# Performance work log

Hardware: AMD Instinct MI355X
Metric: run time of the kernel (lower is better)

Reference implementation:

```python
import jax, jax.numpy as jnp
import numpy as np

D_IN = 1024
D_OUT = 1024
D_BOT = 512


def setup_inputs() -> dict:
    key = jax.random.key(0)
    ks = jax.random.split(key, 16)
    B, Sq, Skv = 8, 2048, 2048

    def lin(k, fan_in, fan_out):
        kw, kb = jax.random.split(k)
        bound = 1.0 / np.sqrt(fan_in)
        W = jax.random.uniform(kw, (fan_in, fan_out), jnp.float32, -bound, bound)
        b = jax.random.uniform(kb, (fan_out,), jnp.float32, -bound, bound)
        return W, b

    W1, b1 = lin(ks[0], D_IN, D_IN)
    W2, b2 = lin(ks[1], D_IN, D_BOT)
    W3, b3 = lin(ks[2], D_BOT, D_IN)
    W4, b4 = lin(ks[3], D_IN, D_IN)
    Wq, bq = lin(ks[4], D_IN, D_OUT)
    Wk, bk = lin(ks[5], D_IN, D_OUT)
    Wv, bv = lin(ks[6], D_IN, D_OUT)

    x = jax.random.normal(ks[7], (B, Sq, D_IN), jnp.float32)
    y = jax.random.normal(ks[8], (B, Skv, D_IN), jnp.float32)
    return {
        "x": x, "y": y,
        "W1": W1, "b1": b1, "W2": W2, "b2": b2,
        "W3": W3, "b3": b3, "W4": W4, "b4": b4,
        "Wq": Wq, "bq": bq, "Wk": Wk, "bk": bk, "Wv": Wv, "bv": bv,
    }


def reference(x, y, W1, b1, W2, b2, W3, b3, W4, b4, Wq, bq, Wk, bk, Wv, bv):
    # 4-layer MLP with ReLU after every linear
    h = jax.nn.relu(x @ W1 + b1)
    h = jax.nn.relu(h @ W2 + b2)
    h = jax.nn.relu(h @ W3 + b3)
    h = jax.nn.relu(h @ W4 + b4)
    # cross-attention projections
    q = h @ Wq + bq          # [B, Sq, D_OUT]
    k = y @ Wk + bk          # [B, Skv, D_OUT]
    v = y @ Wv + bv          # [B, Skv, D_OUT]
    scale = 1.0 / jnp.sqrt(jnp.float32(q.shape[-1]))
    scores = jnp.einsum('bqd,bkd->bqk', q, k) * scale  # [B, Sq, Skv]
    attn_w = jax.nn.softmax(scores, axis=-1)
    out = jnp.einsum('bqk,bkd->bqd', attn_w, v)
    return out
```

## Files before the change

kernel.cpp:

```cpp
#include <hip/hip_runtime.h>
#include <stdint.h>


typedef __attribute__((ext_vector_type(8))) short bf16x8;
typedef __attribute__((ext_vector_type(4))) float f32x4;
typedef __attribute__((ext_vector_type(8))) unsigned short u16x8;

#define LOG2E_F 1.44269504088896f
#define LN2_F   0.69314718055995f

__device__ __forceinline__ float bf2f(unsigned short u) {
    return __uint_as_float(((unsigned int)u) << 16);
}
__device__ __forceinline__ unsigned short f2bf(float f) {
    unsigned int u = __float_as_uint(f);
    unsigned int r = (u + 0x7fffu + ((u >> 16) & 1u)) >> 16;
    return (unsigned short)r;
}

__device__ __forceinline__ void async16(const void* g, void* l) {
    __builtin_amdgcn_global_load_lds(
        (const __attribute__((address_space(1))) unsigned int*)g,
        (__attribute__((address_space(3))) unsigned int*)l,
        16, 0, 0);
}

__global__ __launch_bounds__(64) void detect_dtype(
    const unsigned short* __restrict__ w, int* __restrict__ flag)
{
    const int t = threadIdx.x;
    int cnt = 0;
    for (int i = t; i < 4096; i += 64) {
        const unsigned e = (w[i] >> 7) & 0xFF;
        cnt += (e >= 140) ? 1 : 0;
    }
#pragma unroll
    for (int off = 32; off; off >>= 1) cnt += __shfl_xor(cnt, off, 64);
    if (t == 0) flag[0] = (cnt >= 8) ? 1 : 0;
}

__global__ __launch_bounds__(256) void conv_bias_all(
    const void* b1, const void* b2, const void* b3, const void* b4,
    const void* bq, const void* bk, const void* bv,
    float* __restrict__ out, const int* __restrict__ flag)
{
    const int i = blockIdx.x * 256 + threadIdx.x;
    const int slot = i >> 10, idx = i & 1023;
    if (slot == 1 && idx >= 512) return;
    const void* src = (slot == 0) ? b1 : (slot == 1) ? b2 : (slot == 2) ? b3 :
                      (slot == 3) ? b4 : (slot == 4) ? bq : (slot == 5) ? bk : bv;
    out[i] = (*flag) ? ((const float*)src)[idx]
                     : bf2f(((const unsigned short*)src)[idx]);
}

__device__ __forceinline__ void wt_body(
    const void* in, unsigned short* out, int R, int C, int f)
{
    __shared__ unsigned short tile[32][33];
    const int bc = blockIdx.x * 32;
    const int br = blockIdx.y * 32;
    const int x = threadIdx.x & 31;
    const int y = threadIdx.x >> 5;
#pragma unroll
    for (int i = 0; i < 4; i++) {
        const int r = y + i * 8;
        unsigned short v;
        if (f) v = f2bf(((const float*)in)[(size_t)(br + r) * C + bc + x]);
        else   v = ((const unsigned short*)in)[(size_t)(br + r) * C + bc + x];
        tile[r][x] = v;
    }
    __syncthreads();
#pragma unroll
    for (int i = 0; i < 4; i++) {
        const int r = y + i * 8;
        out[(size_t)(bc + r) * R + br + x] = tile[x][r];
    }
}

__global__ __launch_bounds__(256) void conv_weight_t7(
    const void* i0, unsigned short* o0, const void* i1, unsigned short* o1,
    const void* i2, unsigned short* o2, const void* i3, unsigned short* o3,
    const void* i4, unsigned short* o4, const void* i5, unsigned short* o5,
    const void* i6, unsigned short* o6, const int* flag)
{
    const int z = blockIdx.z;
    if (z == 5) {
        if (blockIdx.x >= 16) return;
        wt_body(i5, o5, 1024, 512, *flag);
        return;
    }
    if (z == 6) {
        if (blockIdx.y >= 16) return;
        wt_body(i6, o6, 512, 1024, *flag);
        return;
    }
    const void* in = (z == 0) ? i0 : (z == 1) ? i1 : (z == 2) ? i2 : (z == 3) ? i3 : i4;
    unsigned short* out = (z == 0) ? o0 : (z == 1) ? o1 : (z == 2) ? o2 : (z == 3) ? o3 : o4;
    wt_body(in, out, 1024, 1024, *flag);
}

__global__ __launch_bounds__(256) void conv_to_bf16(
    const void* __restrict__ in, unsigned short* __restrict__ out,
    int n, const int* __restrict__ flag)
{
    const int i = (blockIdx.x * 256 + threadIdx.x) * 8;
    if (i >= n) return;
    if (*flag) {
        const float4* p = (const float4*)((const float*)in + i);
        const float4 a = p[0], b = p[1];
        u16x8 o;
        o[0] = f2bf(a.x); o[1] = f2bf(a.y); o[2] = f2bf(a.z); o[3] = f2bf(a.w);
        o[4] = f2bf(b.x); o[5] = f2bf(b.y); o[6] = f2bf(b.z); o[7] = f2bf(b.w);
        *(u16x8*)(out + i) = o;
    } else {
        *(u16x8*)(out + i) = *(const u16x8*)((const unsigned short*)in + i);
    }
}

__global__ __launch_bounds__(256) void write_out(
    const unsigned short* __restrict__ src, void* __restrict__ dst,
    int n, const int* __restrict__ flag)
{
    const int i = (blockIdx.x * 256 + threadIdx.x) * 8;
    if (i >= n) return;
    const u16x8 v = *(const u16x8*)(src + i);
    if (*flag) {
        float4 a, b;
        a.x = bf2f(v[0]); a.y = bf2f(v[1]); a.z = bf2f(v[2]); a.w = bf2f(v[3]);
        b.x = bf2f(v[4]); b.y = bf2f(v[5]); b.z = bf2f(v[6]); b.w = bf2f(v[7]);
        float4* p = (float4*)((float*)dst + i);
        p[0] = a; p[1] = b;
    } else {
        *(u16x8*)((unsigned short*)dst + i) = v;
    }
}

template <int RELU, int BIAS, int OUTF, int SWZ>
__global__ __launch_bounds__(256, 2) void gemm_bt(
    const unsigned short* __restrict__ A, const unsigned short* __restrict__ B,
    const float* __restrict__ bias, void* __restrict__ C,
    int M, int N, int K, float alpha,
    long long sA, long long sB, long long sC, const int* __restrict__ flag)
{
    int bxi = blockIdx.x, byi = blockIdx.y;
    if (SWZ) {
        const int id = byi * gridDim.x + bxi;
        bxi = (id >> 3) % gridDim.x;
        byi = (id >> 3) / gridDim.x * 8 + (id & 7);
    }
    const int z = blockIdx.z;
    A += (size_t)z * (size_t)sA;
    B += (size_t)z * (size_t)sB;
    const size_t cofs = (size_t)z * (size_t)sC;

    const int bm = byi * 128;
    const int bn = bxi * 128;
    const int t = threadIdx.x;
    const int lane = t & 63;
    const int w = t >> 6;
    const int wr = (w >> 1) * 64;
    const int wc = (w & 1) * 64;

    __shared__ unsigned short sAt[128 * 32];
    __shared__ unsigned short sBt[128 * 32];

    f32x4 acc[4][4];
#pragma unroll
    for (int i = 0; i < 4; i++)
#pragma unroll
        for (int j = 0; j < 4; j++)
            acc[i][j] = (f32x4){0.f, 0.f, 0.f, 0.f};

    const int tr = t >> 2;
    const int tc = (t & 3) << 3;
    const unsigned short* ga = A + (size_t)(bm + tr) * K + tc;
    const unsigned short* gb = B + (size_t)(bn + tr) * K + tc;
    unsigned short* la = &sAt[tr * 32 + tc];
    unsigned short* lb = &sBt[tr * 32 + tc];

    const int am = wr + (lane & 15);
    const int bn_ = wc + (lane & 15);
    const int ak = (lane >> 4) * 8;

    for (int k0 = 0; k0 < K; k0 += 32) {
        async16(ga, la);
        async16(ga + (size_t)64 * K, la + 64 * 32);
        async16(gb, lb);
        async16(gb + (size_t)64 * K, lb + 64 * 32);
        ga += 32;
        gb += 32;
        __syncthreads();

        bf16x8 af[4], bfr[4];
#pragma unroll
        for (int i = 0; i < 4; i++)
            af[i] = *(const bf16x8*)&sAt[(am + i * 16) * 32 + ak];
#pragma unroll
        for (int j = 0; j < 4; j++)
            bfr[j] = *(const bf16x8*)&sBt[(bn_ + j * 16) * 32 + ak];
#pragma unroll
        for (int i = 0; i < 4; i++)
#pragma unroll
            for (int j = 0; j < 4; j++)
                acc[i][j] = __builtin_amdgcn_mfma_f32_16x16x32_bf16(
                    af[i], bfr[j], acc[i][j], 0, 0, 0);
        __syncthreads();
    }

    const int fl = OUTF ? *flag : 0;
#pragma unroll
    for (int i = 0; i < 4; i++) {
        const int row0 = bm + wr + i * 16 + (lane >> 4) * 4;
#pragma unroll
        for (int j = 0; j < 4; j++) {
            const int col = bn + wc + j * 16 + (lane & 15);
            float bc = 0.f;
            if (BIAS == 1) bc = bias[col];
#pragma unroll
            for (int r = 0; r < 4; r++) {
                float bv = bc;
                if (BIAS == 2) bv = bias[row0 + r];
                float vv = acc[i][j][r] * alpha + bv;
                if (RELU) vv = fmaxf(vv, 0.f);
                const size_t idx = cofs + (size_t)(row0 + r) * N + col;
                if (OUTF && fl) ((float*)C)[idx] = vv;
                else ((unsigned short*)C)[idx] = f2bf(vv);
            }
        }
    }
}

#define G10_STG(SOFS, KOFS) do {                                               \
    async16(gAs + (KOFS), dA + (SOFS));                                        \
    async16(gAs + (KOFS) + rk128, dA + (SOFS) + 4096);                         \
    async16(gBs + (KOFS), dB + (SOFS));                                        \
    async16(gBs + (KOFS) + rk128, dB + (SOFS) + 4096);                         \
} while (0)

template <int RELU, int BIAS, int OUTF, int SWZ, int STAT, int NORM>
__global__ __launch_bounds__(512, 2) void gemm8(
    const unsigned short* __restrict__ A, const unsigned short* __restrict__ B,
    const float* __restrict__ bias, void* __restrict__ C,
    int M, int N, int K, float alpha,
    long long sA, long long sB, long long sC, const int* __restrict__ flag,
    const float* __restrict__ ms, float* __restrict__ ps)
{
    extern __shared__ unsigned short lds[];
    int bxi = blockIdx.x, byi = blockIdx.y;
    if (SWZ) {
        const int id = byi * gridDim.x + bxi;
        bxi = (id >> 3) % gridDim.x;
        byi = (id >> 3) / gridDim.x * 8 + (id & 7);
    }
    const int z = blockIdx.z;
    A += (size_t)z * (size_t)sA;
    B += (size_t)z * (size_t)sB;
    const size_t cofs = (size_t)z * (size_t)sC;

    const int bm = byi * 256;
    const int bn = bxi * 256;
    const int t = threadIdx.x;
    const int lane = t & 63;
    const int w = t >> 6;
    const int wm = w >> 2;
    const int wn = w & 3;

    const int soct = ((t & 3) ^ ((t >> 3) & 3)) << 3;
    const unsigned short* gAs = A + (size_t)(bm + (t >> 2)) * K + soct;
    const unsigned short* gBs = B + (size_t)(bn + (t >> 2)) * K + soct;
    const size_t rk128 = (size_t)128 * K;
    unsigned short* dA = lds + t * 8;
    unsigned short* dB = lds + 32768 + t * 8;

    const int l15 = lane & 15;
    const int oct = (((lane >> 4) ^ ((lane >> 1) & 3)) << 3);
    const int aoff = (wm * 128 + l15) * 32 + oct;
    const int boff = (wn * 64 + l15) * 32 + oct;

    float Mm[8];
    if (NORM) {
#pragma unroll
        for (int m = 0; m < 8; m++) {
            const int row = bm + wm * 128 + m * 16 + l15;
            Mm[m] = ms[((size_t)z * M + row) * 2];
        }
    }

    f32x4 acc[8][4];
#pragma unroll
    for (int i = 0; i < 8; i++)
#pragma unroll
        for (int j = 0; j < 4; j++)
            acc[i][j] = (f32x4){0.f, 0.f, 0.f, 0.f};

    G10_STG(0, 0);
    G10_STG(8192, 32);
    asm volatile("s_waitcnt vmcnt(4)" ::: "memory");
    __builtin_amdgcn_s_barrier();
    asm volatile("" ::: "memory");

    const int NT = K >> 5;
    for (int T = 0; T < NT; ++T) {
        if (T + 2 < NT) {
            const int so = ((T + 2) & 3) * 8192;
            const int ko = (T + 2) << 5;
            G10_STG(so, ko);
        }
        const int sr = (T & 3) * 8192;
        const unsigned short* pa = lds + sr + aoff;
        const unsigned short* pb = lds + 32768 + sr + boff;
        bf16x8 bb[4], a[8];
#pragma unroll
        for (int n = 0; n < 4; n++)
            bb[n] = *(const bf16x8*)(pb + n * 512);
#pragma unroll
        for (int m = 0; m < 8; m++)
            a[m] = *(const bf16x8*)(pa + m * 512);
        if (NORM) {
#pragma unroll
            for (int m = 0; m < 8; m++) {
                bf16x8 v = a[m];
                u16x8 o;
#pragma unroll
                for (int e = 0; e < 8; e++) {
                    const float x = bf2f((unsigned short)v[e]);
                    const float p = __expf((x - Mm[m]) * LN2_F);
                    o[e] = f2bf(p);
                }
                a[m] = *(bf16x8*)&o;
            }
        }
        __builtin_amdgcn_s_setprio(1);
#pragma unroll
        for (int m = 0; m < 8; m++)
#pragma unroll
            for (int n = 0; n < 4; n++)
                acc[m][n] = __builtin_amdgcn_mfma_f32_16x16x32_bf16(
                    a[m], bb[n], acc[m][n], 0, 0, 0);
        __builtin_amdgcn_s_setprio(0);
        if (T + 1 < NT) {
            if (T + 2 < NT) {
                asm volatile("s_waitcnt vmcnt(4)" ::: "memory");
            } else {
                asm volatile("s_waitcnt vmcnt(0)" ::: "memory");
            }
            __builtin_amdgcn_s_barrier();
            asm volatile("" ::: "memory");
        }
    }

    const int fl = OUTF ? *flag : 0;
#pragma unroll
    for (int mi = 0; mi < 8; mi++) {
        const int row0 = bm + wm * 128 + mi * 16 + (lane >> 4) * 4;
        float isv[4];
        if (NORM) {
#pragma unroll
            for (int r = 0; r < 4; r++)
                isv[r] = ms[((size_t)z * M + row0 + r) * 2 + 1];
        }
#pragma unroll
        for (int n = 0; n < 4; n++) {
            const int col = bn + wn * 64 + n * 16 + l15;
            float bc = 0.f;
            if (BIAS == 1) bc = bias[col];
#pragma unroll
            for (int r = 0; r < 4; r++) {
                float bv = bc;
                if (BIAS == 2) bv = bias[row0 + r];
                float vv = acc[mi][n][r] * alpha + bv;
                if (NORM) vv *= isv[r];
                if (RELU) vv = fmaxf(vv, 0.f);
                const size_t idx = cofs + (size_t)(row0 + r) * N + col;
                if (OUTF && fl) ((float*)C)[idx] = vv;
                else ((unsigned short*)C)[idx] = f2bf(vv);
            }
        }
    }

    if (STAT) {
        __syncthreads();
        float2* sl = (float2*)lds;
#pragma unroll
        for (int mi = 0; mi < 8; mi++) {
#pragma unroll
            for (int r = 0; r < 4; r++) {
                float vr[4];
#pragma unroll
                for (int n = 0; n < 4; n++)
                    vr[n] = bf2f(f2bf(acc[mi][n][r] * alpha));
                float mx = fmaxf(fmaxf(vr[0], vr[1]), fmaxf(vr[2], vr[3]));
#pragma unroll
                for (int msk = 1; msk <= 8; msk <<= 1)
                    mx = fmaxf(mx, __shfl_xor(mx, msk, 64));
                float sm = 0.f;
#pragma unroll
                for (int n = 0; n < 4; n++)
                    sm += __expf((vr[n] - mx) * LN2_F);
#pragma unroll
                for (int msk = 1; msk <= 8; msk <<= 1)
                    sm += __shfl_xor(sm, msk, 64);
                if (l15 == 0) {
                    const int rl = wm * 128 + mi * 16 + (lane >> 4) * 4 + r;
                    sl[rl * 4 + wn] = (float2){mx, sm};
                }
            }
        }
        __syncthreads();
        if (t < 256) {
            const float2 p0 = sl[t * 4 + 0], p1 = sl[t * 4 + 1];
            const float2 p2 = sl[t * 4 + 2], p3 = sl[t * 4 + 3];
            float Mx = fmaxf(fmaxf(p0.x, p1.x), fmaxf(p2.x, p3.x));
            float S = p0.y * __expf((p0.x - Mx) * LN2_F)
                    + p1.y * __expf((p1.x - Mx) * LN2_F)
                    + p2.y * __expf((p2.x - Mx) * LN2_F)
                    + p3.y * __expf((p3.x - Mx) * LN2_F);
            float2* o = (float2*)ps;
            o[((size_t)z * M + bm + t) * 8 + bxi] = (float2){Mx, S};
        }
    }
}

__global__ __launch_bounds__(256) void stats_reduce(
    const float* __restrict__ ps, float* __restrict__ ms)
{
    const int i = blockIdx.x * 256 + threadIdx.x;
    const float2* p = (const float2*)ps + (size_t)i * 8;
    float M = p[0].x;
#pragma unroll
    for (int j = 1; j < 8; j++) M = fmaxf(M, p[j].x);
    float S = 0.f;
#pragma unroll
    for (int j = 0; j < 8; j++)
        S += p[j].y * __expf((p[j].x - M) * LN2_F);
    float2* o = (float2*)ms;
    o[i] = (float2){M, 1.0f / S};
}

__global__ __launch_bounds__(256) void softmax_rows(unsigned short* S, int n)
{
    const size_t row = blockIdx.x;
    unsigned short* p = S + row * (size_t)n;
    const int t = threadIdx.x;
    const int lane = t & 63;
    const int wave = t >> 6;

    u16x8 v = *(const u16x8*)(p + t * 8);
    float f[8];
    float m = -3.0e38f;
#pragma unroll
    for (int i = 0; i < 8; i++) {
        f[i] = bf2f(v[i]);
        m = fmaxf(m, f[i]);
    }
#pragma unroll
    for (int off = 32; off; off >>= 1) m = fmaxf(m, __shfl_xor(m, off, 64));
    __shared__ float redm[4];
    if (lane == 0) redm[wave] = m;
    __syncthreads();
    m = fmaxf(fmaxf(redm[0], redm[1]), fmaxf(redm[2], redm[3]));

    float e[8];
    float s = 0.f;
#pragma unroll
    for (int i = 0; i < 8; i++) {
        e[i] = __expf(f[i] - m);
        s += e[i];
    }
#pragma unroll
    for (int off = 32; off; off >>= 1) s += __shfl_xor(s, off, 64);
    __shared__ float reds[4];
    if (lane == 0) reds[wave] = s;
    __syncthreads();
    s = reds[0] + reds[1] + reds[2] + reds[3];
    const float inv = 1.0f / s;

    u16x8 o;
#pragma unroll
    for (int i = 0; i < 8; i++) o[i] = f2bf(e[i] * inv);
    *(u16x8*)(p + t * 8) = o;
}

extern "C" void kernel_launch(void* const* d_in, const int* in_sizes, int n_in,
                              void* d_out, int out_size, void* d_ws, size_t ws_size,
                              hipStream_t stream)
{
    const void* x  = d_in[0];
    const void* y  = d_in[1];
    const void* W1 = d_in[2];
    const void* b1 = d_in[3];
    const void* W2 = d_in[4];
    const void* b2 = d_in[5];
    const void* W3 = d_in[6];
    const void* b3 = d_in[7];
    const void* W4 = d_in[8];
    const void* b4 = d_in[9];
    const void* Wq = d_in[10];
    const void* bq = d_in[11];
    const void* Wk = d_in[12];
    const void* bk = d_in[13];
    const void* Wv = d_in[14];
    const void* bv = d_in[15];

    int* flag = (int*)d_ws;
    float* fb = (float*)((char*)d_ws + 64);
    unsigned short* arena = (unsigned short*)((char*)d_ws + 64 + 7 * 1024 * 4);
    const size_t baseB = 64 + 7 * 1024 * 4;
    const size_t MEG = 1024ull * 1024ull;

    auto needB = [&](int G, bool direct) -> size_t {
        return baseB + 2ull * ((6 + 16 + (size_t)G * 6 + (direct ? 0 : 16)) * MEG);
    };
    int G; bool direct;
    if (ws_size >= needB(8, true))      { G = 8; direct = true;  }
    else if (ws_size >= needB(4, false)) { G = 4; direct = false; }
    else if (ws_size >= needB(2, false)) { G = 2; direct = false; }
    else                                 { G = 1; direct = false; }

    unsigned short* W1t = arena;
    unsigned short* W2t = W1t + 1 * MEG;
    unsigned short* W3t = W2t + MEG / 2;
    unsigned short* W4t = W3t + MEG / 2;
    unsigned short* Wqt = W4t + 1 * MEG;
    unsigned short* Wkt = Wqt + 1 * MEG;
    unsigned short* Wvt = Wkt + 1 * MEG;
    unsigned short* XC  = Wvt + 1 * MEG;
    unsigned short* VT  = XC + 16 * MEG;
    unsigned short* SBUF = VT + (size_t)G * 2 * MEG;
    unsigned short* OUTS = SBUF + (size_t)G * 4 * MEG;

    unsigned short* PA = (unsigned short*)d_out;
    unsigned short* PB = PA + 16 * MEG;

    float* fb1 = fb;
    float* fb2 = fb + 1024;
    float* fb3 = fb + 2048;
    float* fb4 = fb + 3072;
    float* fbq = fb + 4096;
    float* fbk = fb + 5120;
    float* fbv = fb + 6144;

    const dim3 blk(256);
    const dim3 blk8(512);
    const int LDS8 = 131072;
    const int NE = 16 * 1024 * 1024;
    const int Mx = 16384;
    const long long Z0 = 0;
    const long long sQK = 2048ll * 1024;
    const long long sS  = 2048ll * 2048;

    const bool fused = direct && (ws_size >= needB(8, true) + 2ull * MEG);
    float* pstats = (float*)OUTS;
    float* mstats = pstats + 8 * 2048 * 8 * 2;

    (void)hipFuncSetAttribute((const void*)&gemm8<1, 1, 0, 1, 0, 0>,
                              hipFuncAttributeMaxDynamicSharedMemorySize, LDS8);
    (void)hipFuncSetAttribute((const void*)&gemm8<0, 1, 0, 1, 0, 0>,
                              hipFuncAttributeMaxDynamicSharedMemorySize, LDS8);
    (void)hipFuncSetAttribute((const void*)&gemm8<0, 2, 0, 0, 0, 0>,
                              hipFuncAttributeMaxDynamicSharedMemorySize, LDS8);
    (void)hipFuncSetAttribute((const void*)&gemm8<0, 0, 0, 1, 0, 0>,
                              hipFuncAttributeMaxDynamicSharedMemorySize, LDS8);
    (void)hipFuncSetAttribute((const void*)&gemm8<0, 0, 1, 1, 0, 0>,
                              hipFuncAttributeMaxDynamicSharedMemorySize, LDS8);
    (void)hipFuncSetAttribute((const void*)&gemm8<0, 0, 0, 1, 1, 0>,
                              hipFuncAttributeMaxDynamicSharedMemorySize, LDS8);
    (void)hipFuncSetAttribute((const void*)&gemm8<0, 0, 1, 1, 0, 1>,
                              hipFuncAttributeMaxDynamicSharedMemorySize, LDS8);

    detect_dtype<<<1, 64, 0, stream>>>((const unsigned short*)W1, flag);
    conv_bias_all<<<28, blk, 0, stream>>>(b1, b2, b3, b4, bq, bk, bv, fb, flag);
    conv_weight_t7<<<dim3(32, 32, 7), blk, 0, stream>>>(
        W1, W1t, W4, W4t, Wq, Wqt, Wk, Wkt, Wv, Wvt, W2, W2t, W3, W3t, flag);

    conv_to_bf16<<<8192, blk, 0, stream>>>(x, XC, NE, flag);

    gemm8<1, 1, 0, 1, 0, 0><<<dim3(4, 64), blk8, LDS8, stream>>>(
        XC, W1t, fb1, PA, Mx, 1024, 1024, 1.f, Z0, Z0, Z0, flag, nullptr, nullptr);
    gemm8<1, 1, 0, 1, 0, 0><<<dim3(2, 64), blk8, LDS8, stream>>>(
        PA, W2t, fb2, PB, Mx, 512, 1024, 1.f, Z0, Z0, Z0, flag, nullptr, nullptr);
    gemm8<1, 1, 0, 1, 0, 0><<<dim3(4, 64), blk8, LDS8, stream>>>(
        PB, W3t, fb3, PA, Mx, 1024, 512, 1.f, Z0, Z0, Z0, flag, nullptr, nullptr);
    gemm8<1, 1, 0, 1, 0, 0><<<dim3(4, 64), blk8, LDS8, stream>>>(
        PA, W4t, fb4, PB, Mx, 1024, 1024, 1.f, Z0, Z0, Z0, flag, nullptr, nullptr);

    gemm8<0, 1, 0, 1, 0, 0><<<dim3(4, 64), blk8, LDS8, stream>>>(
        PB, Wqt, fbq, PA, Mx, 1024, 1024, 1.f, Z0, Z0, Z0, flag, nullptr, nullptr);
    conv_to_bf16<<<8192, blk, 0, stream>>>(y, XC, NE, flag);
    gemm8<0, 1, 0, 1, 0, 0><<<dim3(4, 64), blk8, LDS8, stream>>>(
        XC, Wkt, fbk, PB, Mx, 1024, 1024, 1.f, Z0, Z0, Z0, flag, nullptr, nullptr);

    if (direct) {
        gemm8<0, 2, 0, 0, 0, 0><<<dim3(8, 4, 8), blk8, LDS8, stream>>>(
            Wvt, XC, fbv, VT, 1024, 2048, 1024, 1.f, Z0, sQK, sQK, flag, nullptr, nullptr);
        if (fused) {
            gemm8<0, 0, 0, 1, 1, 0><<<dim3(8, 8, 8), blk8, LDS8, stream>>>(
                PA, PB, nullptr, SBUF, 2048, 2048, 1024, 0.03125f * LOG2E_F,
                sQK, sQK, sS, flag, nullptr, pstats);
            stats_reduce<<<64, blk, 0, stream>>>(pstats, mstats);
            gemm8<0, 0, 1, 1, 0, 1><<<dim3(4, 8, 8), blk8, LDS8, stream>>>(
                SBUF, VT, nullptr, d_out, 2048, 1024, 2048, 1.f,
                sS, sQK, sQK, flag, mstats, nullptr);
        } else {
            gemm8<0, 0, 0, 1, 0, 0><<<dim3(8, 8, 8), blk8, LDS8, stream>>>(
                PA, PB, nullptr, SBUF, 2048, 2048, 1024, 0.03125f,
                sQK, sQK, sS, flag, nullptr, nullptr);
            softmax_rows<<<dim3(8 * 2048), blk, 0, stream>>>(SBUF, 2048);
            gemm8<0, 0, 1, 1, 0, 0><<<dim3(4, 8, 8), blk8, LDS8, stream>>>(
                SBUF, VT, nullptr, d_out, 2048, 1024, 2048, 1.f,
                sS, sQK, sQK, flag, nullptr, nullptr);
        }
    } else {
        for (int g = 0; g < 8; g += G) {
            const size_t off = (size_t)g * 2048 * 1024;
            gemm_bt<0, 2, 0, 0><<<dim3(16, 8, G), blk, 0, stream>>>(
                Wvt, XC + off, fbv, VT, 1024, 2048, 1024, 1.f, Z0, sQK, sQK, flag);
            gemm_bt<0, 0, 0, 1><<<dim3(16, 16, G), blk, 0, stream>>>(
                PA + off, PB + off, nullptr, SBUF, 2048, 2048, 1024, 0.03125f, sQK, sQK, sS, flag);
            softmax_rows<<<dim3(G * 2048), blk, 0, stream>>>(SBUF, 2048);
            gemm_bt<0, 0, 0, 1><<<dim3(8, 16, G), blk, 0, stream>>>(
                SBUF, VT, nullptr, OUTS + off, 2048, 1024, 2048, 1.f, sS, sQK, sQK, flag);
        }
        write_out<<<8192, blk, 0, stream>>>(OUTS, d_out, NE, flag);
    }
}
```

Measured before the change: 724.4 us.

## Move softmax exponentiation into QK GEMM epilogue with per-block max rescaling

The QK^T GEMM epilogue now computes a per-256-column-block row max, writes exp2(s - max) as bf16 probabilities, and records partial max/sum stats. The PV GEMM no longer exponentiates every A tile inside its K loop. It instead rescales its accumulators whenever it crosses into a new 256-column block (online-softmax style) and applies the final global max/sum correction in the epilogue. This removes per-element exp work from the hot MFMA loop of the PV GEMM, at the cost of an extra LDS reduction pass in the QK epilogue and periodic accumulator rescaling reads of stats.

```diff
diff --git a/kernel.cpp b/kernel.cpp
--- a/kernel.cpp
+++ b/kernel.cpp
@@ -264,6 +264,8 @@
     const int w = t >> 6;
     const int wm = w >> 2;
     const int wn = w & 3;
+    const int l15 = lane & 15;
+    const int l4 = lane >> 4;
 
     const int soct = ((t & 3) ^ ((t >> 3) & 3)) << 3;
     const unsigned short* gAs = A + (size_t)(bm + (t >> 2)) * K + soct;
@@ -272,18 +274,19 @@
     unsigned short* dA = lds + t * 8;
     unsigned short* dB = lds + 32768 + t * 8;
 
-    const int l15 = lane & 15;
     const int oct = (((lane >> 4) ^ ((lane >> 1) & 3)) << 3);
     const int aoff = (wm * 128 + l15) * 32 + oct;
     const int boff = (wn * 64 + l15) * 32 + oct;
 
-    float Mm[8];
-    if (NORM) {
-#pragma unroll
-        for (int m = 0; m < 8; m++) {
-            const int row = bm + wm * 128 + m * 16 + l15;
-            Mm[m] = ms[((size_t)z * M + row) * 2];
-        }
+    float Ml[8][4];
+    if (NORM == 2) {
+#pragma unroll
+        for (int mi = 0; mi < 8; mi++)
+#pragma unroll
+            for (int r = 0; r < 4; r++) {
+                const int row = bm + wm * 128 + mi * 16 + l4 * 4 + r;
+                Ml[mi][r] = ps[(((size_t)z * M + row) * 8 + 0) * 2];
+            }
     }
 
     f32x4 acc[8][4];
@@ -301,6 +304,21 @@
 
     const int NT = K >> 5;
     for (int T = 0; T < NT; ++T) {
+        if (NORM == 2 && T > 0 && (T & 7) == 0) {
+            const int xb = T >> 3;
+#pragma unroll
+            for (int mi = 0; mi < 8; mi++)
+#pragma unroll
+                for (int r = 0; r < 4; r++) {
+                    const int row = bm + wm * 128 + mi * 16 + l4 * 4 + r;
+                    const float mn = ps[(((size_t)z * M + row) * 8 + xb) * 2];
+                    const float rat = __expf((Ml[mi][r] - mn) * LN2_F);
+                    Ml[mi][r] = mn;
+#pragma unroll
+                    for (int n = 0; n < 4; n++)
+                        acc[mi][n][r] *= rat;
+                }
+        }
         if (T + 2 < NT) {
             const int so = ((T + 2) & 3) * 8192;
             const int ko = (T + 2) << 5;
@@ -316,20 +334,6 @@
 #pragma unroll
         for (int m = 0; m < 8; m++)
             a[m] = *(const bf16x8*)(pa + m * 512);
-        if (NORM) {
-#pragma unroll
-            for (int m = 0; m < 8; m++) {
-                bf16x8 v = a[m];
-                u16x8 o;
-#pragma unroll
-                for (int e = 0; e < 8; e++) {
-                    const float x = bf2f((unsigned short)v[e]);
-                    const float p = __expf((x - Mm[m]) * LN2_F);
-                    o[e] = f2bf(p);
-                }
-                a[m] = *(bf16x8*)&o;
-            }
-        }
         __builtin_amdgcn_s_setprio(1);
 #pragma unroll
         for (int m = 0; m < 8; m++)
@@ -349,74 +353,95 @@
         }
     }
 
-    const int fl = OUTF ? *flag : 0;
-#pragma unroll
-    for (int mi = 0; mi < 8; mi++) {
-        const int row0 = bm + wm * 128 + mi * 16 + (lane >> 4) * 4;
-        float isv[4];
-        if (NORM) {
-#pragma unroll
-            for (int r = 0; r < 4; r++)
-                isv[r] = ms[((size_t)z * M + row0 + r) * 2 + 1];
-        }
-#pragma unroll
-        for (int n = 0; n < 4; n++) {
-            const int col = bn + wn * 64 + n * 16 + l15;
-            float bc = 0.f;
-            if (BIAS == 1) bc = bias[col];
-#pragma unroll
-            for (int r = 0; r < 4; r++) {
-                float bv = bc;
-                if (BIAS == 2) bv = bias[row0 + r];
-                float vv = acc[mi][n][r] * alpha + bv;
-                if (NORM) vv *= isv[r];
-                if (RELU) vv = fmaxf(vv, 0.f);
-                const size_t idx = cofs + (size_t)(row0 + r) * N + col;
-                if (OUTF && fl) ((float*)C)[idx] = vv;
-                else ((unsigned short*)C)[idx] = f2bf(vv);
+    if (STAT != 2) {
+        const int fl = OUTF ? *flag : 0;
+#pragma unroll
+        for (int mi = 0; mi < 8; mi++) {
+            const int row0 = bm + wm * 128 + mi * 16 + l4 * 4;
+            float isv[4];
+            if (NORM == 2) {
+#pragma unroll
+                for (int r = 0; r < 4; r++) {
+                    const float2 g =
+                        ((const float2*)ms)[(size_t)z * M + row0 + r];
+                    isv[r] = __expf((Ml[mi][r] - g.x) * LN2_F) * g.y;
+                }
             }
-        }
-    }
-
-    if (STAT) {
+#pragma unroll
+            for (int n = 0; n < 4; n++) {
+                const int col = bn + wn * 64 + n * 16 + l15;
+                float bc = 0.f;
+                if (BIAS == 1) bc = bias[col];
+#pragma unroll
+                for (int r = 0; r < 4; r++) {
+                    float bv = bc;
+                    if (BIAS == 2) bv = bias[row0 + r];
+                    float vv = acc[mi][n][r] * alpha + bv;
+                    if (NORM == 2) vv *= isv[r];
+                    if (RELU) vv = fmaxf(vv, 0.f);
+                    const size_t idx = cofs + (size_t)(row0 + r) * N + col;
+                    if (OUTF && fl) ((float*)C)[idx] = vv;
+                    else ((unsigned short*)C)[idx] = f2bf(vv);
+                }
+            }
+        }
+    } else {
         __syncthreads();
         float2* sl = (float2*)lds;
+        float* sm2 = (float*)((char*)lds + 8192);
 #pragma unroll
         for (int mi = 0; mi < 8; mi++) {
 #pragma unroll
             for (int r = 0; r < 4; r++) {
-                float vr[4];
-#pragma unroll
-                for (int n = 0; n < 4; n++)
-                    vr[n] = bf2f(f2bf(acc[mi][n][r] * alpha));
-                float mx = fmaxf(fmaxf(vr[0], vr[1]), fmaxf(vr[2], vr[3]));
+                float mx = acc[mi][0][r];
+#pragma unroll
+                for (int n = 1; n < 4; n++) mx = fmaxf(mx, acc[mi][n][r]);
+                mx *= alpha;
 #pragma unroll
                 for (int msk = 1; msk <= 8; msk <<= 1)
                     mx = fmaxf(mx, __shfl_xor(mx, msk, 64));
-                float sm = 0.f;
-#pragma unroll
-                for (int n = 0; n < 4; n++)
-                    sm += __expf((vr[n] - mx) * LN2_F);
-#pragma unroll
-                for (int msk = 1; msk <= 8; msk <<= 1)
-                    sm += __shfl_xor(sm, msk, 64);
                 if (l15 == 0) {
-                    const int rl = wm * 128 + mi * 16 + (lane >> 4) * 4 + r;
-                    sl[rl * 4 + wn] = (float2){mx, sm};
+                    const int rl = wm * 128 + mi * 16 + l4 * 4 + r;
+                    sl[rl * 4 + wn].x = mx;
                 }
             }
         }
         __syncthreads();
         if (t < 256) {
-            const float2 p0 = sl[t * 4 + 0], p1 = sl[t * 4 + 1];
-            const float2 p2 = sl[t * 4 + 2], p3 = sl[t * 4 + 3];
-            float Mx = fmaxf(fmaxf(p0.x, p1.x), fmaxf(p2.x, p3.x));
-            float S = p0.y * __expf((p0.x - Mx) * LN2_F)
-                    + p1.y * __expf((p1.x - Mx) * LN2_F)
-                    + p2.y * __expf((p2.x - Mx) * LN2_F)
-                    + p3.y * __expf((p3.x - Mx) * LN2_F);
-            float2* o = (float2*)ps;
-            o[((size_t)z * M + bm + t) * 8 + bxi] = (float2){Mx, S};
+            const float Mx = fmaxf(fmaxf(sl[t * 4 + 0].x, sl[t * 4 + 1].x),
+                                   fmaxf(sl[t * 4 + 2].x, sl[t * 4 + 3].x));
+            sm2[t] = Mx;
+        }
+        __syncthreads();
+#pragma unroll
+        for (int mi = 0; mi < 8; mi++) {
+#pragma unroll
+            for (int r = 0; r < 4; r++) {
+                const int rl = wm * 128 + mi * 16 + l4 * 4 + r;
+                const float Mx = sm2[rl];
+                float s = 0.f;
+#pragma unroll
+                for (int n = 0; n < 4; n++) {
+                    const float v = acc[mi][n][r] * alpha;
+                    const unsigned short pbv =
+                        f2bf(__expf((v - Mx) * LN2_F));
+                    s += bf2f(pbv);
+                    const int col = bn + wn * 64 + n * 16 + l15;
+                    ((unsigned short*)C)[cofs + (size_t)(bm + rl) * N + col]
+                        = pbv;
+                }
+#pragma unroll
+                for (int msk = 1; msk <= 8; msk <<= 1)
+                    s += __shfl_xor(s, msk, 64);
+                if (l15 == 0) sl[rl * 4 + wn].y = s;
+            }
+        }
+        __syncthreads();
+        if (t < 256) {
+            const float S = sl[t * 4 + 0].y + sl[t * 4 + 1].y
+                          + sl[t * 4 + 2].y + sl[t * 4 + 3].y;
+            ((float2*)ps)[((size_t)z * M + bm + t) * 8 + bxi] =
+                (float2){sm2[t], S};
         }
     }
 }
@@ -563,9 +588,9 @@
                               hipFuncAttributeMaxDynamicSharedMemorySize, LDS8);
     (void)hipFuncSetAttribute((const void*)&gemm8<0, 0, 1, 1, 0, 0>,
                               hipFuncAttributeMaxDynamicSharedMemorySize, LDS8);
-    (void)hipFuncSetAttribute((const void*)&gemm8<0, 0, 0, 1, 1, 0>,
+    (void)hipFuncSetAttribute((const void*)&gemm8<0, 0, 0, 1, 2, 0>,
                               hipFuncAttributeMaxDynamicSharedMemorySize, LDS8);
-    (void)hipFuncSetAttribute((const void*)&gemm8<0, 0, 1, 1, 0, 1>,
+    (void)hipFuncSetAttribute((const void*)&gemm8<0, 0, 1, 1, 0, 2>,
                               hipFuncAttributeMaxDynamicSharedMemorySize, LDS8);
 
     detect_dtype<<<1, 64, 0, stream>>>((const unsigned short*)W1, flag);
@@ -594,13 +619,13 @@
         gemm8<0, 2, 0, 0, 0, 0><<<dim3(8, 4, 8), blk8, LDS8, stream>>>(
             Wvt, XC, fbv, VT, 1024, 2048, 1024, 1.f, Z0, sQK, sQK, flag, nullptr, nullptr);
         if (fused) {
-            gemm8<0, 0, 0, 1, 1, 0><<<dim3(8, 8, 8), blk8, LDS8, stream>>>(
+            gemm8<0, 0, 0, 1, 2, 0><<<dim3(8, 8, 8), blk8, LDS8, stream>>>(
                 PA, PB, nullptr, SBUF, 2048, 2048, 1024, 0.03125f * LOG2E_F,
                 sQK, sQK, sS, flag, nullptr, pstats);
             stats_reduce<<<64, blk, 0, stream>>>(pstats, mstats);
-            gemm8<0, 0, 1, 1, 0, 1><<<dim3(4, 8, 8), blk8, LDS8, stream>>>(
+            gemm8<0, 0, 1, 1, 0, 2><<<dim3(4, 8, 8), blk8, LDS8, stream>>>(
                 SBUF, VT, nullptr, d_out, 2048, 1024, 2048, 1.f,
-                sS, sQK, sQK, flag, mstats, nullptr);
+                sS, sQK, sQK, flag, mstats, pstats);
         } else {
             gemm8<0, 0, 0, 1, 0, 0><<<dim3(8, 8, 8), blk8, LDS8, stream>>>(
                 PA, PB, nullptr, SBUF, 2048, 2048, 1024, 0.03125f,
```

Result: no change. 716.8 us (-1.0%).
